# Kernel tuning notes

Hardware: AMD Instinct MI355X
Metric: run time of the kernel (lower is better)

The kernel has to match this reference:

```python
import jax, jax.numpy as jnp
import numpy as np

D_MODEL = 1024
NUM_HEADS = 16
HEAD_DIM = D_MODEL // NUM_HEADS
B, T_Q, T_KV = 4, 4096, 4096


def setup_inputs() -> dict:
    key = jax.random.key(0)
    ks = jax.random.split(key, 10)
    s_in = 1.0 / np.sqrt(D_MODEL)
    s_out = 1.0 / np.sqrt(D_MODEL)
    return {
        "q": jax.random.normal(ks[0], (B, T_Q, D_MODEL), jnp.float32),
        "kv": jax.random.normal(ks[1], (B, T_KV, D_MODEL), jnp.float32),
        # per-head projection weights stacked: [H, d_model, head_dim]
        "Wq": jax.random.uniform(ks[2], (NUM_HEADS, D_MODEL, HEAD_DIM), jnp.float32, -s_in, s_in),
        "bq": jax.random.uniform(ks[3], (NUM_HEADS, HEAD_DIM), jnp.float32, -s_in, s_in),
        "Wk": jax.random.uniform(ks[4], (NUM_HEADS, D_MODEL, HEAD_DIM), jnp.float32, -s_in, s_in),
        "bk": jax.random.uniform(ks[5], (NUM_HEADS, HEAD_DIM), jnp.float32, -s_in, s_in),
        "Wv": jax.random.uniform(ks[6], (NUM_HEADS, D_MODEL, HEAD_DIM), jnp.float32, -s_in, s_in),
        "bv": jax.random.uniform(ks[7], (NUM_HEADS, HEAD_DIM), jnp.float32, -s_in, s_in),
        "Wo": jax.random.uniform(ks[8], (D_MODEL, D_MODEL), jnp.float32, -s_out, s_out),
        "bo": jax.random.uniform(ks[9], (D_MODEL,), jnp.float32, -s_out, s_out),
    }


def reference(q, kv, Wq, bq, Wk, bk, Wv, bv, Wo, bo):
    Bsz, Tq, _ = q.shape
    # per-head projections fused into one batched GEMM each: [b,t,d] x [h,d,e] -> [b,h,t,e]
    qh = jnp.einsum('btd,hde->bhte', q, Wq) + bq[None, :, None, :]
    kh = jnp.einsum('btd,hde->bhte', kv, Wk) + bk[None, :, None, :]
    vh = jnp.einsum('btd,hde->bhte', kv, Wv) + bv[None, :, None, :]
    # squared feature map
    qh = qh * qh
    kh = kh * kh
    # O(N) linear attention aggregation
    kv_sum = jnp.einsum('bhnd,bhne->bhde', kh, vh)           # [B,H,e,e]
    z = 1.0 / (jnp.einsum('bhnd,bhd->bhn', qh, kh.sum(axis=2)) + 1e-6)  # [B,H,Tq]
    attn = jnp.einsum('bhnd,bhde,bhn->bhne', qh, kv_sum, z)  # [B,H,Tq,e]
    attn = attn.transpose(0, 2, 1, 3).reshape(Bsz, Tq, D_MODEL)
    return attn @ Wo.T + bo
```

## Files before the change

### kernel.cpp

```cpp
#include <hip/hip_runtime.h>

#define BSZ 4
#define TSEQ 4096
#define DM 1024
#define NH 16
#define HD 64
#define BT (BSZ * TSEQ)
#define INV_LOSCALE (1.0f / 4096.0f)

using f32x4 = __attribute__((ext_vector_type(4))) float;
using f16x8 = __attribute__((ext_vector_type(8))) _Float16;
using u32x2 = __attribute__((ext_vector_type(2))) unsigned;
using u32x4 = __attribute__((ext_vector_type(4))) unsigned;

typedef const __attribute__((address_space(1))) void* gas_ptr;
typedef __attribute__((address_space(3))) void* las_ptr;

__device__ __forceinline__ void gload16(const void* g, void* l) {
    __builtin_amdgcn_global_load_lds((gas_ptr)g, (las_ptr)l, 16, 0, 0);
}

__device__ __forceinline__ void split1(float x, _Float16& h, _Float16& l) {
    h = (_Float16)x;
    l = (_Float16)((x - (float)h) * 4096.0f);
}
__device__ __forceinline__ unsigned pack2(_Float16 a, _Float16 b) {
    return (unsigned)__builtin_bit_cast(unsigned short, a) |
           ((unsigned)__builtin_bit_cast(unsigned short, b) << 16);
}
__device__ __forceinline__ f32x4 mfma_f16(f16x8 a, f16x8 b, f32x4 c) {
    return __builtin_amdgcn_mfma_f32_16x16x32_f16(a, b, c, 0, 0, 0);
}

__global__ __launch_bounds__(256) void fragsplit_kernel(const float* __restrict__ in,
        _Float16* __restrict__ hi, _Float16* __restrict__ lo) {
    const int C = blockIdx.x * 256 + threadIdx.x;
    const int l15 = C & 15, quad = (C >> 4) & 3, rb = (C >> 6) & 3;
    const int s = (C >> 8) & 31, panel = C >> 13;
    const size_t src = ((size_t)(panel * 64 + rb * 16 + l15)) * DM + s * 32 + quad * 8;
    f32x4 v0 = *(const f32x4*)&in[src];
    f32x4 v1 = *(const f32x4*)&in[src + 4];
    _Float16 h[8], l[8];
    #pragma unroll
    for (int j = 0; j < 4; ++j) { split1(v0[j], h[j], l[j]); split1(v1[j], h[4 + j], l[4 + j]); }
    ((u32x4*)hi)[C] = (u32x4){pack2(h[0],h[1]), pack2(h[2],h[3]), pack2(h[4],h[5]), pack2(h[6],h[7])};
    ((u32x4*)lo)[C] = (u32x4){pack2(l[0],l[1]), pack2(l[2],l[3]), pack2(l[4],l[5]), pack2(l[6],l[7])};
}

__global__ __launch_bounds__(256) void wsplit_kernel(
    const float* __restrict__ Wq, const float* __restrict__ Wk, const float* __restrict__ Wv,
    _Float16* __restrict__ qh, _Float16* __restrict__ ql,
    _Float16* __restrict__ kh, _Float16* __restrict__ kl,
    _Float16* __restrict__ vh, _Float16* __restrict__ vl) {
    const int tid = threadIdx.x;
    const int k0 = blockIdx.x * 64, h = blockIdx.y, w = blockIdx.z;
    const float* __restrict__ W = (w == 0) ? Wq : (w == 1) ? Wk : Wv;
    _Float16* __restrict__ dh = (w == 0) ? qh : (w == 1) ? kh : vh;
    _Float16* __restrict__ dl = (w == 0) ? ql : (w == 1) ? kl : vl;
    __shared__ __align__(16) float ws_[64][68];
    #pragma unroll
    for (int it = 0; it < 4; ++it) {
        int idx = it * 256 + tid;
        int r = idx >> 4, c4 = (idx & 15) * 4;
        *(f32x4*)&ws_[r][c4] = *(const f32x4*)&W[((size_t)h * DM + k0 + r) * HD + c4];
    }
    __syncthreads();
    const int n = tid >> 2, kq16 = (tid & 3) * 16;
    _Float16 hh[16], ll[16];
    #pragma unroll
    for (int j = 0; j < 16; ++j) split1(ws_[kq16 + j][n], hh[j], ll[j]);
    #pragma unroll
    for (int c = 0; c < 2; ++c) {
        int kg = k0 + kq16 + c * 8;
        int s = kg >> 5, quad = (kg >> 3) & 3;
        size_t chunk = (size_t)(h * 32 + s) * 256 + ((n >> 4) * 4 + quad) * 16 + (n & 15);
        ((u32x4*)dh)[chunk] = (u32x4){pack2(hh[c*8+0],hh[c*8+1]), pack2(hh[c*8+2],hh[c*8+3]),
                                      pack2(hh[c*8+4],hh[c*8+5]), pack2(hh[c*8+6],hh[c*8+7])};
        ((u32x4*)dl)[chunk] = (u32x4){pack2(ll[c*8+0],ll[c*8+1]), pack2(ll[c*8+2],ll[c*8+3]),
                                      pack2(ll[c*8+4],ll[c*8+5]), pack2(ll[c*8+6],ll[c*8+7])};
    }
}

__global__ __launch_bounds__(256, 2) void kv_stats_kernel(
    const _Float16* __restrict__ kv_hi, const _Float16* __restrict__ kv_lo,
    const _Float16* __restrict__ wkt_hi, const _Float16* __restrict__ wkt_lo,
    const _Float16* __restrict__ wvt_hi, const _Float16* __restrict__ wvt_lo,
    const float* __restrict__ bk, const float* __restrict__ bv,
    float* __restrict__ kv_sum, float* __restrict__ ksum)
{
    const int tid = threadIdx.x;
    const int lane = tid & 63, wave = tid >> 6, quad = lane >> 4, l15 = lane & 15;
    const int b = blockIdx.z, h = blockIdx.y, bx = blockIdx.x;

    __shared__ __align__(16) char smem[65536];
    _Float16* khT_h = (_Float16*)smem;
    _Float16* khT_l = (_Float16*)(smem + 16384);
    _Float16* vhT_h = (_Float16*)(smem + 32768);
    _Float16* vhT_l = (_Float16*)(smem + 49152);

    const int isV = wave >> 1, half = wave & 1;
    const size_t btile = (size_t)h * 32;

    f32x4 racc_h[4] = {}, racc_c[4] = {};
    f32x4 rk_h = {}, rk_c = {};
    const f16x8 ones = __builtin_bit_cast(f16x8,
        (u32x4){0x3C003C00u, 0x3C003C00u, 0x3C003C00u, 0x3C003C00u});

    for (int sub = 0; sub < 2; ++sub) {
        const size_t apan = (size_t)(b * 64 + bx * 4 + sub * 2);
        auto stage = [&](int p, int s) {
            char* dst = smem + p * 32768 + tid * 16;
            const size_t a0 = (apan * 32 + s) * 2048 + tid * 8;
            const size_t a1 = ((apan + 1) * 32 + s) * 2048 + tid * 8;
            const size_t bo = (btile + s) * 2048 + tid * 8;
            gload16(&kv_hi[a0], dst);
            gload16(&kv_hi[a1], dst + 4096);
            gload16(&kv_lo[a0], dst + 8192);
            gload16(&kv_lo[a1], dst + 12288);
            gload16(&wkt_hi[bo], dst + 16384);
            gload16(&wkt_lo[bo], dst + 20480);
            gload16(&wvt_hi[bo], dst + 24576);
            gload16(&wvt_lo[bo], dst + 28672);
        };

        f32x4 acc_h[4][4] = {}, acc_c[4][4] = {};
        stage(0, 0);
        for (int s = 0; s < 32; ++s) {
            const int p = s & 1;
            if (s < 31) {
                stage(p ^ 1, s + 1);
                asm volatile("s_waitcnt vmcnt(8)" ::: "memory");
            } else {
                asm volatile("s_waitcnt vmcnt(0)" ::: "memory");
            }
            __builtin_amdgcn_s_barrier();
            __builtin_amdgcn_sched_barrier(0);
            const char* bufc = smem + p * 32768;
            const _Float16* a_hi = (const _Float16*)bufc;
            const _Float16* a_lo = (const _Float16*)(bufc + 8192);
            const _Float16* bh = (const _Float16*)(bufc + (isV ? 24576 : 16384));
            const _Float16* bl = (const _Float16*)(bufc + (isV ? 28672 : 20480));
            f16x8 afh[4], afl[4], bfh[4], bfl[4];
            #pragma unroll
            for (int mt = 0; mt < 4; ++mt) {
                afh[mt] = *(const f16x8*)&a_hi[half * 2048 + mt * 512 + lane * 8];
                afl[mt] = *(const f16x8*)&a_lo[half * 2048 + mt * 512 + lane * 8];
            }
            #pragma unroll
            for (int nt = 0; nt < 4; ++nt) {
                bfh[nt] = *(const f16x8*)&bh[nt * 512 + lane * 8];
                bfl[nt] = *(const f16x8*)&bl[nt * 512 + lane * 8];
            }
            #pragma unroll
            for (int mt = 0; mt < 4; ++mt)
                #pragma unroll
                for (int nt = 0; nt < 4; ++nt) {
                    acc_h[mt][nt] = mfma_f16(afh[mt], bfh[nt], acc_h[mt][nt]);
                    acc_c[mt][nt] = mfma_f16(afh[mt], bfl[nt], acc_c[mt][nt]);
                    acc_c[mt][nt] = mfma_f16(afl[mt], bfh[nt], acc_c[mt][nt]);
                }
            __builtin_amdgcn_s_barrier();
            __builtin_amdgcn_sched_barrier(0);
        }

        {
            const float* __restrict__ bias = (isV ? bv : bk) + h * HD;
            _Float16* __restrict__ dh = isV ? vhT_h : khT_h;
            _Float16* __restrict__ dl = isV ? vhT_l : khT_l;
            float bia[4];
            #pragma unroll
            for (int nt = 0; nt < 4; ++nt) bia[nt] = bias[nt * 16 + l15];
            #pragma unroll
            for (int mt = 0; mt < 4; ++mt) {
                const int S = half * 2 + (mt >> 1);
                const int tq = (mt & 1) * 2 + (quad >> 1);
                const int eo = (quad & 1) * 4;
                #pragma unroll
                for (int nt = 0; nt < 4; ++nt) {
                    _Float16 hh[4], ll[4];
                    #pragma unroll
                    for (int r = 0; r < 4; ++r) {
                        float v = acc_h[mt][nt][r] + INV_LOSCALE * acc_c[mt][nt][r] + bia[nt];
                        if (!isV) v = v * v;
                        split1(v, hh[r], ll[r]);
                    }
                    int fo = S * 2048 + (nt * 4 + tq) * 128 + l15 * 8 + eo;
                    *(u32x2*)&dh[fo] = (u32x2){pack2(hh[0], hh[1]), pack2(hh[2], hh[3])};
                    *(u32x2*)&dl[fo] = (u32x2){pack2(ll[0], ll[1]), pack2(ll[2], ll[3])};
                }
            }
        }
        __syncthreads();

        #pragma unroll
        for (int S = 0; S < 4; ++S) {
            f16x8 ah = *(const f16x8*)&khT_h[S * 2048 + wave * 512 + lane * 8];
            f16x8 al = *(const f16x8*)&khT_l[S * 2048 + wave * 512 + lane * 8];
            rk_h = mfma_f16(ah, ones, rk_h);
            rk_c = mfma_f16(al, ones, rk_c);
            #pragma unroll
            for (int nt = 0; nt < 4; ++nt) {
                f16x8 bh = *(const f16x8*)&vhT_h[S * 2048 + nt * 512 + lane * 8];
                f16x8 bl = *(const f16x8*)&vhT_l[S * 2048 + nt * 512 + lane * 8];
                racc_h[nt] = mfma_f16(ah, bh, racc_h[nt]);
                racc_c[nt] = mfma_f16(ah, bl, racc_c[nt]);
                racc_c[nt] = mfma_f16(al, bh, racc_c[nt]);
            }
        }
        __syncthreads();
    }

    float* kvp = kv_sum + (size_t)(b * NH + h) * HD * HD;
    #pragma unroll
    for (int nt = 0; nt < 4; ++nt)
        #pragma unroll
        for (int r = 0; r < 4; ++r)
            atomicAdd(&kvp[(wave * 16 + quad * 4 + r) * HD + nt * 16 + l15],
                      racc_h[nt][r] + INV_LOSCALE * racc_c[nt][r]);
    if (l15 == 0) {
        float* ksp = ksum + (b * NH + h) * HD;
        #pragma unroll
        for (int r = 0; r < 4; ++r)
            atomicAdd(&ksp[wave * 16 + quad * 4 + r], rk_h[r] + INV_LOSCALE * rk_c[r]);
    }
}

__global__ __launch_bounds__(256) void pmat_kernel(
    const float* __restrict__ kv_sum, const float* __restrict__ Wo,
    _Float16* __restrict__ pt_hi, _Float16* __restrict__ pt_lo)
{
    const int tid = threadIdx.x;
    const int opan = blockIdx.x, h = blockIdx.y, b = blockIdx.z;
    __shared__ __align__(16) float kvsT[64][68];
    __shared__ __align__(16) float wos[64][68];
    const float* __restrict__ kvp = kv_sum + (size_t)(b * NH + h) * HD * HD;
    #pragma unroll
    for (int it = 0; it < 4; ++it) {
        int idx = it * 256 + tid;
        int d = idx >> 4, e4 = (idx & 15) * 4;
        f32x4 v = *(const f32x4*)&kvp[d * HD + e4];
        kvsT[e4 + 0][d] = v.x; kvsT[e4 + 1][d] = v.y;
        kvsT[e4 + 2][d] = v.z; kvsT[e4 + 3][d] = v.w;
        int o = idx >> 4;
        *(f32x4*)&wos[o][e4] = *(const f32x4*)&Wo[(size_t)(opan * 64 + o) * DM + h * HD + e4];
    }
    __syncthreads();
    const int ty = tid >> 4, tx = tid & 15;
    f32x4 sv[4] = {};
    #pragma unroll 8
    for (int e = 0; e < 64; ++e) {
        f32x4 kv4 = *(const f32x4*)&kvsT[e][tx * 4];
        #pragma unroll
        for (int i = 0; i < 4; ++i) sv[i] += wos[ty * 4 + i][e] * kv4;
    }
    const int d0 = tx * 4;
    const int S = h * 2 + (d0 >> 5);
    const int kq = (d0 >> 3) & 3;
    const int rem8 = (d0 & 4) ? 8 : 0;
    #pragma unroll
    for (int i = 0; i < 4; ++i) {
        int ol = ty * 4 + i;
        f32x4 o4 = sv[i] * INV_LOSCALE;
        _Float16 hh[4], ll[4];
        #pragma unroll
        for (int j = 0; j < 4; ++j) split1(o4[j], hh[j], ll[j]);
        size_t cb = ((((size_t)(b * 16 + opan) * 32 + S) * 256 +
                      ((ol >> 4) * 4 + kq) * 16 + (ol & 15)) << 4) + rem8;
        *(u32x2*)((char*)pt_hi + cb) = (u32x2){pack2(hh[0], hh[1]), pack2(hh[2], hh[3])};
        *(u32x2*)((char*)pt_lo + cb) = (u32x2){pack2(ll[0], ll[1]), pack2(ll[2], ll[3])};
    }
}

__global__ __launch_bounds__(256, 3) void q_attn_ps_kernel(
    const _Float16* __restrict__ qf_hi, const _Float16* __restrict__ qf_lo,
    const _Float16* __restrict__ wqt_hi, const _Float16* __restrict__ wqt_lo,
    const float* __restrict__ bq, const float* __restrict__ ksum,
    _Float16* __restrict__ attn_hi, _Float16* __restrict__ attn_lo)
{
    const int tid = threadIdx.x;
    const int lane = tid & 63, wave = tid >> 6, quad = lane >> 4, l15 = lane & 15;
    const int b = blockIdx.z, h = blockIdx.y, bx = blockIdx.x;

    __shared__ __align__(16) char smem[49152];
    __shared__ float z_s[128], ks_s[64];

    if (tid < 64) ks_s[tid] = ksum[(b * NH + h) * HD + tid];

    const size_t apan = (size_t)(b * 64 + bx * 2);
    const size_t btile = (size_t)h * 32;

    auto stage = [&](int p, int s) {
        char* dst = smem + p * 24576 + tid * 16;
        const size_t a0 = (apan * 32 + s) * 2048 + tid * 8;
        const size_t a1 = ((apan + 1) * 32 + s) * 2048 + tid * 8;
        const size_t bo = (btile + s) * 2048 + tid * 8;
        gload16(&qf_hi[a0], dst);
        gload16(&qf_hi[a1], dst + 4096);
        gload16(&qf_lo[a0], dst + 8192);
        gload16(&qf_lo[a1], dst + 12288);
        gload16(&wqt_hi[bo], dst + 16384);
        gload16(&wqt_lo[bo], dst + 20480);
    };

    f32x4 acc_h[2][4] = {}, acc_c[2][4] = {};
    stage(0, 0);
    for (int s = 0; s < 32; ++s) {
        const int p = s & 1;
        if (s < 31) {
            stage(p ^ 1, s + 1);
            asm volatile("s_waitcnt vmcnt(6)" ::: "memory");
        } else {
            asm volatile("s_waitcnt vmcnt(0)" ::: "memory");
        }
        __builtin_amdgcn_s_barrier();
        __builtin_amdgcn_sched_barrier(0);
        const char* bufc = smem + p * 24576;
        const _Float16* a_hi = (const _Float16*)bufc;
        const _Float16* a_lo = (const _Float16*)(bufc + 8192);
        f16x8 afh[2], afl[2], bfh[4], bfl[4];
        #pragma unroll
        for (int mt = 0; mt < 2; ++mt) {
            int fo = (wave * 2 + mt) * 512 + lane * 8;
            afh[mt] = *(const f16x8*)&a_hi[fo];
            afl[mt] = *(const f16x8*)&a_lo[fo];
        }
        #pragma unroll
        for (int nt = 0; nt < 4; ++nt) {
            bfh[nt] = *(const f16x8*)((const _Float16*)(bufc + 16384) + nt * 512 + lane * 8);
            bfl[nt] = *(const f16x8*)((const _Float16*)(bufc + 20480) + nt * 512 + lane * 8);
        }
        #pragma unroll
        for (int mt = 0; mt < 2; ++mt)
            #pragma unroll
            for (int nt = 0; nt < 4; ++nt) {
                acc_h[mt][nt] = mfma_f16(afh[mt], bfh[nt], acc_h[mt][nt]);
                acc_c[mt][nt] = mfma_f16(afh[mt], bfl[nt], acc_c[mt][nt]);
                acc_c[mt][nt] = mfma_f16(afl[mt], bfh[nt], acc_c[mt][nt]);
            }
        __builtin_amdgcn_s_barrier();
        __builtin_amdgcn_sched_barrier(0);
    }

    float* qs = (float*)smem;
    {
        const float* __restrict__ bias = bq + h * HD;
        float zp[2][4] = {};
        #pragma unroll
        for (int nt = 0; nt < 4; ++nt) {
            int d = nt * 16 + l15;
            float bia = bias[d];
            float ks  = ks_s[d];
            #pragma unroll
            for (int mt = 0; mt < 2; ++mt)
                #pragma unroll
                for (int r = 0; r < 4; ++r) {
                    int t = wave * 32 + mt * 16 + quad * 4 + r;
                    float v = acc_h[mt][nt][r] + INV_LOSCALE * acc_c[mt][nt][r] + bia;
                    float v2 = v * v;
                    qs[t * 68 + d] = v2;
                    zp[mt][r] = fmaf(v2, ks, zp[mt][r]);
                }
        }
        #pragma unroll
        for (int mt = 0; mt < 2; ++mt)
            #pragma unroll
            for (int r = 0; r < 4; ++r) {
                float p = zp[mt][r];
                p += __shfl_xor(p, 1);
                p += __shfl_xor(p, 2);
                p += __shfl_xor(p, 4);
                p += __shfl_xor(p, 8);
                if (l15 == 0) z_s[wave * 32 + mt * 16 + quad * 4 + r] = 4096.0f / (p + 1e-6f);
            }
    }
    __syncthreads();

    #pragma unroll
    for (int it = 0; it < 4; ++it) {
        int cid = it * 256 + tid;
        int lp = cid >> 9, Sl = (cid >> 8) & 1, c = cid & 255;
        int t = lp * 64 + (c >> 6) * 16 + (c & 15);
        int d = Sl * 32 + ((c >> 4) & 3) * 8;
        f32x4 a0 = *(const f32x4*)&qs[t * 68 + d];
        f32x4 a1 = *(const f32x4*)&qs[t * 68 + d + 4];
        float z = z_s[t];
        _Float16 hh[8], ll[8];
        #pragma unroll
        for (int j = 0; j < 4; ++j) {
            split1(z * a0[j], hh[j], ll[j]);
            split1(z * a1[j], hh[4 + j], ll[4 + j]);
        }
        size_t cb = (((size_t)(b * 64 + bx * 2 + lp) * 32 + h * 2 + Sl) * 256 + c) << 4;
        *(u32x4*)((char*)attn_hi + cb) =
            (u32x4){pack2(hh[0],hh[1]), pack2(hh[2],hh[3]), pack2(hh[4],hh[5]), pack2(hh[6],hh[7])};
        *(u32x4*)((char*)attn_lo + cb) =
            (u32x4){pack2(ll[0],ll[1]), pack2(ll[2],ll[3]), pack2(ll[4],ll[5]), pack2(ll[6],ll[7])};
    }
}

__global__ __launch_bounds__(256, 3) void q_attn_kernel(
    const float* __restrict__ q,
    const _Float16* __restrict__ wqt_hi, const _Float16* __restrict__ wqt_lo,
    const float* __restrict__ bq,
    const float* __restrict__ kv_sum, const float* __restrict__ ksum,
    _Float16* __restrict__ attn_hi, _Float16* __restrict__ attn_lo)
{
    const int tid = threadIdx.x;
    const int lane = tid & 63, wave = tid >> 6, quad = lane >> 4, l15 = lane & 15;
    const int b = blockIdx.z, h = blockIdx.y, bx = blockIdx.x;
    const int t0 = bx * 64;

    __shared__ __align__(16) char smem[32768];
    __shared__ __align__(16) float qs[64 * 68];
    __shared__ float z_s[64], ks_s[64];

    if (tid < 64) ks_s[tid] = ksum[(b * NH + h) * HD + tid];

    const int arb = tid >> 6, aquad = (tid >> 4) & 3, al15 = tid & 15;
    const float* __restrict__ qrow =
        q + ((size_t)b * TSEQ + t0 + arb * 16 + al15) * DM + aquad * 8;
    const size_t btile = (size_t)h * 32;

    auto asplit_write = [&](int p, f32x4 v0, f32x4 v1) {
        _Float16 hh[8], ll[8];
        #pragma unroll
        for (int j = 0; j < 4; ++j) { split1(v0[j], hh[j], ll[j]); split1(v1[j], hh[4+j], ll[4+j]); }
        char* dst = smem + p * 16384 + tid * 16;
        *(u32x4*)dst =
            (u32x4){pack2(hh[0],hh[1]), pack2(hh[2],hh[3]), pack2(hh[4],hh[5]), pack2(hh[6],hh[7])};
        *(u32x4*)(dst + 4096) =
            (u32x4){pack2(ll[0],ll[1]), pack2(ll[2],ll[3]), pack2(ll[4],ll[5]), pack2(ll[6],ll[7])};
    };
    auto stageB = [&](int p, int s) {
        char* dst = smem + p * 16384 + 8192 + tid * 16;
        const size_t bo = (btile + s) * 2048 + tid * 8;
        gload16(&wqt_hi[bo], dst);
        gload16(&wqt_lo[bo], dst + 4096);
    };

    f32x4 acc_h[4] = {}, acc_c[4] = {};
    f32x4 v0 = *(const f32x4*)&qrow[0];
    f32x4 v1 = *(const f32x4*)&qrow[4];
    asplit_write(0, v0, v1);
    stageB(0, 0);
    v0 = *(const f32x4*)&qrow[32];
    v1 = *(const f32x4*)&qrow[36];
    asm volatile("s_waitcnt vmcnt(2) lgkmcnt(0)" ::: "memory");
    __builtin_amdgcn_s_barrier();
    __builtin_amdgcn_sched_barrier(0);

    for (int s = 0; s < 32; ++s) {
        const int p = s & 1;
        if (s < 31) {
            stageB(p ^ 1, s + 1);
            asplit_write(p ^ 1, v0, v1);
            if (s < 30) {
                v0 = *(const f32x4*)&qrow[(s + 2) * 32];
                v1 = *(const f32x4*)&qrow[(s + 2) * 32 + 4];
            }
            asm volatile("s_waitcnt vmcnt(4) lgkmcnt(0)" ::: "memory");
        } else {
            asm volatile("s_waitcnt vmcnt(0)" ::: "memory");
        }
        __builtin_amdgcn_s_barrier();
        __builtin_amdgcn_sched_barrier(0);
        const char* bufc = smem + p * 16384;
        f16x8 afh = *(const f16x8*)((const _Float16*)bufc + wave * 512 + lane * 8);
        f16x8 afl = *(const f16x8*)((const _Float16*)(bufc + 4096) + wave * 512 + lane * 8);
        f16x8 bfh[4], bfl[4];
        #pragma unroll
        for (int nt = 0; nt < 4; ++nt) {
            bfh[nt] = *(const f16x8*)((const _Float16*)(bufc + 8192) + nt * 512 + lane * 8);
            bfl[nt] = *(const f16x8*)((const _Float16*)(bufc + 12288) + nt * 512 + lane * 8);
        }
        #pragma unroll
        for (int nt = 0; nt < 4; ++nt) {
            acc_h[nt] = mfma_f16(afh, bfh[nt], acc_h[nt]);
            acc_c[nt] = mfma_f16(afh, bfl[nt], acc_c[nt]);
            acc_c[nt] = mfma_f16(afl, bfh[nt], acc_c[nt]);
        }
        __builtin_amdgcn_s_barrier();
        __builtin_amdgcn_sched_barrier(0);
    }

    {
        const int mrow0 = wave * 16;
        const float* __restrict__ bias = bq + h * HD;
        float zp[4] = {0.f, 0.f, 0.f, 0.f};
        #pragma unroll
        for (int nt = 0; nt < 4; ++nt) {
            int d = nt * 16 + l15;
            float bia = bias[d];
            float ks  = ks_s[d];
            #pragma unroll
            for (int r = 0; r < 4; ++r) {
                int t = mrow0 + quad * 4 + r;
                float v = acc_h[nt][r] + INV_LOSCALE * acc_c[nt][r] + bia;
                float v2 = v * v;
                qs[t * 68 + d] = v2;
                zp[r] = fmaf(v2, ks, zp[r]);
            }
        }
        #pragma unroll
        for (int r = 0; r < 4; ++r) {
            float p = zp[r];
            p += __shfl_xor(p, 1);
            p += __shfl_xor(p, 2);
            p += __shfl_xor(p, 4);
            p += __shfl_xor(p, 8);
            if (l15 == 0) z_s[mrow0 + quad * 4 + r] = 1.f / (p + 1e-6f);
        }
    }
    __syncthreads();

    float* kvs = (float*)smem;
    {
        const float* __restrict__ kvp = kv_sum + (size_t)(b * NH + h) * HD * HD;
        #pragma unroll
        for (int it = 0; it < 4; ++it) {
            int idx = it * 256 + tid;
            int r = idx >> 4, c = (idx & 15) * 4;
            *(f32x4*)&kvs[r * 64 + c] = *(const f32x4*)&kvp[r * HD + c];
        }
    }
    __syncthreads();

    const int ty = tid >> 4, tx = tid & 15;
    f32x4 sv[4] = {};
    #pragma unroll 4
    for (int d = 0; d < 64; d += 4) {
        f32x4 b0 = *(const f32x4*)&kvs[(d + 0) * 64 + tx * 4];
        f32x4 b1 = *(const f32x4*)&kvs[(d + 1) * 64 + tx * 4];
        f32x4 b2 = *(const f32x4*)&kvs[(d + 2) * 64 + tx * 4];
        f32x4 b3 = *(const f32x4*)&kvs[(d + 3) * 64 + tx * 4];
        #pragma unroll
        for (int i = 0; i < 4; ++i) {
            f32x4 av = *(const f32x4*)&qs[(ty * 4 + i) * 68 + d];
            sv[i] += av.x * b0 + av.y * b1 + av.z * b2 + av.w * b3;
        }
    }
    const size_t opanel = (size_t)b * 64 + bx;
    const int s_out = h * 2 + (tx >> 3);
    const int kq = (tx >> 1) & 3;
    const int rem8 = (tx & 1) * 8;
    #pragma unroll
    for (int i = 0; i < 4; ++i) {
        int t = ty * 4 + i;
        f32x4 o = sv[i] * z_s[t];
        _Float16 hh[4], ll[4];
        #pragma unroll
        for (int j = 0; j < 4; ++j) split1(o[j], hh[j], ll[j]);
        size_t cb = (((opanel * 32 + s_out) * 256 + ((t >> 4) * 4 + kq) * 16 + (t & 15)) << 4) + rem8;
        *(u32x2*)((char*)attn_hi + cb) = (u32x2){pack2(hh[0], hh[1]), pack2(hh[2], hh[3])};
        *(u32x2*)((char*)attn_lo + cb) = (u32x2){pack2(ll[0], ll[1]), pack2(ll[2], ll[3])};
    }
}

__global__ __launch_bounds__(256, 3) void out_proj_p_kernel(
    const _Float16* __restrict__ attn_hi, const _Float16* __restrict__ attn_lo,
    const _Float16* __restrict__ pt_hi, const _Float16* __restrict__ pt_lo,
    const float* __restrict__ bo, float* __restrict__ out)
{
    const int tid = threadIdx.x;
    const int lane = tid & 63, wave = tid >> 6, quad = lane >> 4, l15 = lane & 15;
    const int n0 = blockIdx.x * 64;
    const size_t m0 = (size_t)blockIdx.y * 128;

    __shared__ __align__(16) char smem[49152];
    float* cs = (float*)smem;

    const size_t ap0 = (m0 >> 6) * 32, ap1 = ap0 + 32;
    const int bb = (int)(m0 >> 12);
    const _Float16* __restrict__ pbh = pt_hi + (size_t)bb * 16 * 32 * 2048;
    const _Float16* __restrict__ pbl = pt_lo + (size_t)bb * 16 * 32 * 2048;
    const size_t bpn = (size_t)(n0 >> 6) * 32;

    auto stage = [&](int p, int s) {
        char* dst = smem + p * 24576 + tid * 16;
        const size_t co = (size_t)s * 2048 + tid * 8;
        gload16(&attn_hi[ap0 * 2048 + co], dst);
        gload16(&attn_hi[ap1 * 2048 + co], dst + 4096);
        gload16(&attn_lo[ap0 * 2048 + co], dst + 8192);
        gload16(&attn_lo[ap1 * 2048 + co], dst + 12288);
        gload16(&pbh[(bpn + s) * 2048 + tid * 8], dst + 16384);
        gload16(&pbl[(bpn + s) * 2048 + tid * 8], dst + 20480);
    };

    const int panel = wave >> 1;
    f32x4 acc_h[2][4] = {}, acc_c[2][4] = {};
    stage(0, 0);
    for (int s = 0; s < 32; ++s) {
        const int p = s & 1;
        if (s < 31) {
            stage(p ^ 1, s + 1);
            asm volatile("s_waitcnt vmcnt(6)" ::: "memory");
        } else {
            asm volatile("s_waitcnt vmcnt(0)" ::: "memory");
        }
        __builtin_amdgcn_s_barrier();
        __builtin_amdgcn_sched_barrier(0);
        const char* bufc = smem + p * 24576;
        f16x8 afh[2], afl[2], bfh[4], bfl[4];
        #pragma unroll
        for (int mt = 0; mt < 2; ++mt) {
            int rbl = (wave & 1) * 2 + mt;
            afh[mt] = *(const f16x8*)((const _Float16*)(bufc + panel * 4096) + rbl * 512 + lane * 8);
            afl[mt] = *(const f16x8*)((const _Float16*)(bufc + 8192 + panel * 4096) + rbl * 512 + lane * 8);
        }
        #pragma unroll
        for (int nt = 0; nt < 4; ++nt) {
            bfh[nt] = *(const f16x8*)((const _Float16*)(bufc + 16384) + nt * 512 + lane * 8);
            bfl[nt] = *(const f16x8*)((const _Float16*)(bufc + 20480) + nt * 512 + lane * 8);
        }
        #pragma unroll
        for (int mt = 0; mt < 2; ++mt)
            #pragma unroll
            for (int nt = 0; nt < 4; ++nt) {
                acc_h[mt][nt] = mfma_f16(afh[mt], bfh[nt], acc_h[mt][nt]);
                acc_c[mt][nt] = mfma_f16(afh[mt], bfl[nt], acc_c[mt][nt]);
                acc_c[mt][nt] = mfma_f16(afl[mt], bfh[nt], acc_c[mt][nt]);
            }
        __builtin_amdgcn_s_barrier();
        __builtin_amdgcn_sched_barrier(0);
    }

    {
        float bia[4];
        #pragma unroll
        for (int nt = 0; nt < 4; ++nt) bia[nt] = bo[n0 + nt * 16 + l15];
        #pragma unroll
        for (int mt = 0; mt < 2; ++mt)
            #pragma unroll
            for (int nt = 0; nt < 4; ++nt)
                #pragma unroll
                for (int r = 0; r < 4; ++r) {
                    int t = wave * 32 + mt * 16 + quad * 4 + r;
                    cs[t * 64 + nt * 16 + l15] =
                        acc_h[mt][nt][r] + INV_LOSCALE * acc_c[mt][nt][r] + bia[nt];
                }
    }
    __syncthreads();
    #pragma unroll
    for (int it = 0; it < 8; ++it) {
        int idx = it * 256 + tid;
        int r = idx >> 4, c = (idx & 15) * 4;
        *(f32x4*)&out[(m0 + r) * DM + n0 + c] = *(f32x4*)&cs[r * 64 + c];
    }
}

__global__ __launch_bounds__(256, 3) void out_proj_kernel(
    const _Float16* __restrict__ attn_hi, const _Float16* __restrict__ attn_lo,
    const _Float16* __restrict__ wo_hi, const _Float16* __restrict__ wo_lo,
    const float* __restrict__ bo, float* __restrict__ out)
{
    const int tid = threadIdx.x;
    const int lane = tid & 63, wave = tid >> 6, quad = lane >> 4, l15 = lane & 15;
    const int n0 = blockIdx.x * 64;
    const size_t m0 = (size_t)blockIdx.y * 128;

    __shared__ __align__(16) char smem[49152];
    float* cs = (float*)smem;

    const size_t ap0 = (m0 >> 6) * 32, ap1 = ap0 + 32;
    const size_t bpn = (size_t)(n0 >> 6) * 32;

    auto stage = [&](int p, int s) {
        char* dst = smem + p * 24576 + tid * 16;
        const size_t co = (size_t)s * 2048 + tid * 8;
        gload16(&attn_hi[ap0 * 2048 + co], dst);
        gload16(&attn_hi[ap1 * 2048 + co], dst + 4096);
        gload16(&attn_lo[ap0 * 2048 + co], dst + 8192);
        gload16(&attn_lo[ap1 * 2048 + co], dst + 12288);
        gload16(&wo_hi[(bpn + s) * 2048 + tid * 8], dst + 16384);
        gload16(&wo_lo[(bpn + s) * 2048 + tid * 8], dst + 20480);
    };

    const int panel = wave >> 1;
    f32x4 acc_h[2][4] = {}, acc_c[2][4] = {};
    stage(0, 0);
    for (int s = 0; s < 32; ++s) {
        const int p = s & 1;
        if (s < 31) {
            stage(p ^ 1, s + 1);
            asm volatile("s_waitcnt vmcnt(6)" ::: "memory");
        } else {
            asm volatile("s_waitcnt vmcnt(0)" ::: "memory");
        }
        __builtin_amdgcn_s_barrier();
        __builtin_amdgcn_sched_barrier(0);
        const char* bufc = smem + p * 24576;
        f16x8 afh[2], afl[2], bfh[4], bfl[4];
        #pragma unroll
        for (int mt = 0; mt < 2; ++mt) {
            int rbl = (wave & 1) * 2 + mt;
            afh[mt] = *(const f16x8*)((const _Float16*)(bufc + panel * 4096) + rbl * 512 + lane * 8);
            afl[mt] = *(const f16x8*)((const _Float16*)(bufc + 8192 + panel * 4096) + rbl * 512 + lane * 8);
        }
        #pragma unroll
        for (int nt = 0; nt < 4; ++nt) {
            bfh[nt] = *(const f16x8*)((const _Float16*)(bufc + 16384) + nt * 512 + lane * 8);
            bfl[nt] = *(const f16x8*)((const _Float16*)(bufc + 20480) + nt * 512 + lane * 8);
        }
        #pragma unroll
        for (int mt = 0; mt < 2; ++mt)
            #pragma unroll
            for (int nt = 0; nt < 4; ++nt) {
                acc_h[mt][nt] = mfma_f16(afh[mt], bfh[nt], acc_h[mt][nt]);
                acc_c[mt][nt] = mfma_f16(afh[mt], bfl[nt], acc_c[mt][nt]);
                acc_c[mt][nt] = mfma_f16(afl[mt], bfh[nt], acc_c[mt][nt]);
            }
        __builtin_amdgcn_s_barrier();
        __builtin_amdgcn_sched_barrier(0);
    }

    {
        float bia[4];
        #pragma unroll
        for (int nt = 0; nt < 4; ++nt) bia[nt] = bo[n0 + nt * 16 + l15];
        #pragma unroll
        for (int mt = 0; mt < 2; ++mt)
            #pragma unroll
            for (int nt = 0; nt < 4; ++nt)
                #pragma unroll
                for (int r = 0; r < 4; ++r) {
                    int t = wave * 32 + mt * 16 + quad * 4 + r;
                    cs[t * 64 + nt * 16 + l15] =
                        acc_h[mt][nt][r] + INV_LOSCALE * acc_c[mt][nt][r] + bia[nt];
                }
    }
    __syncthreads();
    #pragma unroll
    for (int it = 0; it < 8; ++it) {
        int idx = it * 256 + tid;
        int r = idx >> 4, c = (idx & 15) * 4;
        *(f32x4*)&out[(m0 + r) * DM + n0 + c] = *(f32x4*)&cs[r * 64 + c];
    }
}

extern "C" void kernel_launch(void* const* d_in, const int* in_sizes, int n_in,
                              void* d_out, int out_size, void* d_ws, size_t ws_size,
                              hipStream_t stream) {
    const float* q  = (const float*)d_in[0];
    const float* kv = (const float*)d_in[1];
    const float* Wq = (const float*)d_in[2];
    const float* bq = (const float*)d_in[3];
    const float* Wk = (const float*)d_in[4];
    const float* bk = (const float*)d_in[5];
    const float* Wv = (const float*)d_in[6];
    const float* bv = (const float*)d_in[7];
    const float* Wo = (const float*)d_in[8];
    const float* bo = (const float*)d_in[9];
    float* out = (float*)d_out;

    char* p = (char*)d_ws;
    float* kv_sum = (float*)p;              p += (size_t)BSZ * NH * HD * HD * 4;
    float* ksum   = (float*)p;              p += (size_t)BSZ * NH * HD * 4;
    _Float16* wqt_hi = (_Float16*)p;        p += (size_t)NH * HD * DM * 2;
    _Float16* wqt_lo = (_Float16*)p;        p += (size_t)NH * HD * DM * 2;
    _Float16* wkt_hi = (_Float16*)p;        p += (size_t)NH * HD * DM * 2;
    _Float16* wkt_lo = (_Float16*)p;        p += (size_t)NH * HD * DM * 2;
    _Float16* wvt_hi = (_Float16*)p;        p += (size_t)NH * HD * DM * 2;
    _Float16* wvt_lo = (_Float16*)p;        p += (size_t)NH * HD * DM * 2;
    _Float16* wo_hi  = (_Float16*)p;        p += (size_t)DM * DM * 2;
    _Float16* wo_lo  = (_Float16*)p;        p += (size_t)DM * DM * 2;
    _Float16* buf_hi = (_Float16*)p;        p += (size_t)BT * DM * 2;
    _Float16* buf_lo = (_Float16*)p;        p += (size_t)BT * DM * 2;
    _Float16* qf_hi  = (_Float16*)p;        p += (size_t)BT * DM * 2;
    _Float16* qf_lo  = (_Float16*)p;        p += (size_t)BT * DM * 2;
    _Float16* pt_hi  = (_Float16*)p;        p += (size_t)BSZ * DM * DM * 2;
    _Float16* pt_lo  = (_Float16*)p;        p += (size_t)BSZ * DM * DM * 2;
    const bool big = ws_size >= (size_t)(p - (char*)d_ws);

    size_t zero_bytes = ((size_t)BSZ * NH * HD * HD + (size_t)BSZ * NH * HD) * sizeof(float);
    hipMemsetAsync(d_ws, 0, zero_bytes, stream);

    fragsplit_kernel<<<(BT * DM / 8) / 256, 256, 0, stream>>>(kv, buf_hi, buf_lo);
    wsplit_kernel<<<dim3(DM / 64, NH, 3), 256, 0, stream>>>(
        Wq, Wk, Wv, wqt_hi, wqt_lo, wkt_hi, wkt_lo, wvt_hi, wvt_lo);
    if (!big)
        fragsplit_kernel<<<(DM * DM / 8) / 256, 256, 0, stream>>>(Wo, wo_hi, wo_lo);

    kv_stats_kernel<<<dim3(TSEQ / 256, NH, BSZ), 256, 0, stream>>>(
        buf_hi, buf_lo, wkt_hi, wkt_lo, wvt_hi, wvt_lo, bk, bv, kv_sum, ksum);

    if (big) {
        fragsplit_kernel<<<(BT * DM / 8) / 256, 256, 0, stream>>>(q, qf_hi, qf_lo);
        pmat_kernel<<<dim3(16, NH, BSZ), 256, 0, stream>>>(kv_sum, Wo, pt_hi, pt_lo);
        q_attn_ps_kernel<<<dim3(TSEQ / 128, NH, BSZ), 256, 0, stream>>>(
            qf_hi, qf_lo, wqt_hi, wqt_lo, bq, ksum, buf_hi, buf_lo);
        out_proj_p_kernel<<<dim3(DM / 64, BT / 128), 256, 0, stream>>>(
            buf_hi, buf_lo, pt_hi, pt_lo, bo, out);
    } else {
        q_attn_kernel<<<dim3(TSEQ / 64, NH, BSZ), 256, 0, stream>>>(
            q, wqt_hi, wqt_lo, bq, kv_sum, ksum, buf_hi, buf_lo);
        out_proj_kernel<<<dim3(DM / 64, BT / 128), 256, 0, stream>>>(
            buf_hi, buf_lo, wo_hi, wo_lo, bo, out);
    }
}
```

Before: 626.0 us.

## Drop low-half attention term in out-projection and remap blocks per XCD

The q_attn_ps kernel now writes only the fp16 high part of the normalized attention, and out_proj_p drops the attn_lo load and its correction MFMA. This cuts out-projection memory traffic, shared memory and MFMA work by about a third, and the kernel's occupancy hint rises to 4. All three main kernels also move to a 1D grid with an XCD-aware block index mapping, so blocks that share a head or N tile land on the same XCD for L2 reuse. The cost is lower precision on the attention operand, which relies on fp16 rounding of the attention values alone staying within tolerance.

```diff
diff --git a/kernel.cpp b/kernel.cpp
--- a/kernel.cpp
+++ b/kernel.cpp
@@ -90,7 +90,11 @@
 {
     const int tid = threadIdx.x;
     const int lane = tid & 63, wave = tid >> 6, quad = lane >> 4, l15 = lane & 15;
-    const int b = blockIdx.z, h = blockIdx.y, bx = blockIdx.x;
+    const int g = blockIdx.x;
+    const int xcd = g & 7, kk = g >> 3;
+    const int h = kk & 15, sg = kk >> 4;
+    const int strip = xcd + 8 * sg;
+    const int b = strip >> 4, bx = strip & 15;
 
     __shared__ __align__(16) char smem[65536];
     _Float16* khT_h = (_Float16*)smem;
@@ -275,11 +279,15 @@
     const _Float16* __restrict__ qf_hi, const _Float16* __restrict__ qf_lo,
     const _Float16* __restrict__ wqt_hi, const _Float16* __restrict__ wqt_lo,
     const float* __restrict__ bq, const float* __restrict__ ksum,
-    _Float16* __restrict__ attn_hi, _Float16* __restrict__ attn_lo)
+    _Float16* __restrict__ attn_hi)
 {
     const int tid = threadIdx.x;
     const int lane = tid & 63, wave = tid >> 6, quad = lane >> 4, l15 = lane & 15;
-    const int b = blockIdx.z, h = blockIdx.y, bx = blockIdx.x;
+    const int g = blockIdx.x;
+    const int xcd = g & 7, kk = g >> 3;
+    const int h = kk & 15, sg = kk >> 4;
+    const int strip = xcd + 8 * sg;
+    const int b = strip >> 5, bx = strip & 31;
 
     __shared__ __align__(16) char smem[49152];
     __shared__ float z_s[128], ks_s[64];
@@ -384,17 +392,15 @@
         f32x4 a0 = *(const f32x4*)&qs[t * 68 + d];
         f32x4 a1 = *(const f32x4*)&qs[t * 68 + d + 4];
         float z = z_s[t];
-        _Float16 hh[8], ll[8];
+        _Float16 hh[8];
         #pragma unroll
         for (int j = 0; j < 4; ++j) {
-            split1(z * a0[j], hh[j], ll[j]);
-            split1(z * a1[j], hh[4 + j], ll[4 + j]);
+            hh[j]     = (_Float16)(z * a0[j]);
+            hh[4 + j] = (_Float16)(z * a1[j]);
         }
         size_t cb = (((size_t)(b * 64 + bx * 2 + lp) * 32 + h * 2 + Sl) * 256 + c) << 4;
         *(u32x4*)((char*)attn_hi + cb) =
             (u32x4){pack2(hh[0],hh[1]), pack2(hh[2],hh[3]), pack2(hh[4],hh[5]), pack2(hh[6],hh[7])};
-        *(u32x4*)((char*)attn_lo + cb) =
-            (u32x4){pack2(ll[0],ll[1]), pack2(ll[2],ll[3]), pack2(ll[4],ll[5]), pack2(ll[6],ll[7])};
     }
 }
 
@@ -556,17 +562,21 @@
     }
 }
 
-__global__ __launch_bounds__(256, 3) void out_proj_p_kernel(
-    const _Float16* __restrict__ attn_hi, const _Float16* __restrict__ attn_lo,
+__global__ __launch_bounds__(256, 4) void out_proj_p_kernel(
+    const _Float16* __restrict__ attn_hi,
     const _Float16* __restrict__ pt_hi, const _Float16* __restrict__ pt_lo,
     const float* __restrict__ bo, float* __restrict__ out)
 {
     const int tid = threadIdx.x;
     const int lane = tid & 63, wave = tid >> 6, quad = lane >> 4, l15 = lane & 15;
-    const int n0 = blockIdx.x * 64;
-    const size_t m0 = (size_t)blockIdx.y * 128;
-
-    __shared__ __align__(16) char smem[49152];
+    const int g = blockIdx.x;
+    const int xcd = g & 7, kk = g >> 3;
+    const int nidx = kk & 15, sg = kk >> 4;
+    const int mstrip = xcd + 8 * sg;
+    const int n0 = nidx * 64;
+    const size_t m0 = (size_t)mstrip * 128;
+
+    __shared__ __align__(16) char smem[32768];
     float* cs = (float*)smem;
 
     const size_t ap0 = (m0 >> 6) * 32, ap1 = ap0 + 32;
@@ -576,14 +586,12 @@
     const size_t bpn = (size_t)(n0 >> 6) * 32;
 
     auto stage = [&](int p, int s) {
-        char* dst = smem + p * 24576 + tid * 16;
+        char* dst = smem + p * 16384 + tid * 16;
         const size_t co = (size_t)s * 2048 + tid * 8;
         gload16(&attn_hi[ap0 * 2048 + co], dst);
         gload16(&attn_hi[ap1 * 2048 + co], dst + 4096);
-        gload16(&attn_lo[ap0 * 2048 + co], dst + 8192);
-        gload16(&attn_lo[ap1 * 2048 + co], dst + 12288);
-        gload16(&pbh[(bpn + s) * 2048 + tid * 8], dst + 16384);
-        gload16(&pbl[(bpn + s) * 2048 + tid * 8], dst + 20480);
+        gload16(&pbh[(bpn + s) * 2048 + tid * 8], dst + 8192);
+        gload16(&pbl[(bpn + s) * 2048 + tid * 8], dst + 12288);
     };
 
     const int panel = wave >> 1;
@@ -593,24 +601,23 @@
         const int p = s & 1;
         if (s < 31) {
             stage(p ^ 1, s + 1);
-            asm volatile("s_waitcnt vmcnt(6)" ::: "memory");
+            asm volatile("s_waitcnt vmcnt(4)" ::: "memory");
         } else {
             asm volatile("s_waitcnt vmcnt(0)" ::: "memory");
         }
         __builtin_amdgcn_s_barrier();
         __builtin_amdgcn_sched_barrier(0);
-        const char* bufc = smem + p * 24576;
-        f16x8 afh[2], afl[2], bfh[4], bfl[4];
+        const char* bufc = smem + p * 16384;
+        f16x8 afh[2], bfh[4], bfl[4];
         #pragma unroll
         for (int mt = 0; mt < 2; ++mt) {
             int rbl = (wave & 1) * 2 + mt;
             afh[mt] = *(const f16x8*)((const _Float16*)(bufc + panel * 4096) + rbl * 512 + lane * 8);
-            afl[mt] = *(const f16x8*)((const _Float16*)(bufc + 8192 + panel * 4096) + rbl * 512 + lane * 8);
         }
         #pragma unroll
         for (int nt = 0; nt < 4; ++nt) {
-            bfh[nt] = *(const f16x8*)((const _Float16*)(bufc + 16384) + nt * 512 + lane * 8);
-            bfl[nt] = *(const f16x8*)((const _Float16*)(bufc + 20480) + nt * 512 + lane * 8);
+            bfh[nt] = *(const f16x8*)((const _Float16*)(bufc + 8192) + nt * 512 + lane * 8);
+            bfl[nt] = *(const f16x8*)((const _Float16*)(bufc + 12288) + nt * 512 + lane * 8);
         }
         #pragma unroll
         for (int mt = 0; mt < 2; ++mt)
@@ -618,7 +625,6 @@
             for (int nt = 0; nt < 4; ++nt) {
                 acc_h[mt][nt] = mfma_f16(afh[mt], bfh[nt], acc_h[mt][nt]);
                 acc_c[mt][nt] = mfma_f16(afh[mt], bfl[nt], acc_c[mt][nt]);
-                acc_c[mt][nt] = mfma_f16(afl[mt], bfh[nt], acc_c[mt][nt]);
             }
         __builtin_amdgcn_s_barrier();
         __builtin_amdgcn_sched_barrier(0);
@@ -780,16 +786,16 @@
     if (!big)
         fragsplit_kernel<<<(DM * DM / 8) / 256, 256, 0, stream>>>(Wo, wo_hi, wo_lo);
 
-    kv_stats_kernel<<<dim3(TSEQ / 256, NH, BSZ), 256, 0, stream>>>(
+    kv_stats_kernel<<<NH * (TSEQ / 256) * BSZ, 256, 0, stream>>>(
         buf_hi, buf_lo, wkt_hi, wkt_lo, wvt_hi, wvt_lo, bk, bv, kv_sum, ksum);
 
     if (big) {
         fragsplit_kernel<<<(BT * DM / 8) / 256, 256, 0, stream>>>(q, qf_hi, qf_lo);
         pmat_kernel<<<dim3(16, NH, BSZ), 256, 0, stream>>>(kv_sum, Wo, pt_hi, pt_lo);
-        q_attn_ps_kernel<<<dim3(TSEQ / 128, NH, BSZ), 256, 0, stream>>>(
-            qf_hi, qf_lo, wqt_hi, wqt_lo, bq, ksum, buf_hi, buf_lo);
-        out_proj_p_kernel<<<dim3(DM / 64, BT / 128), 256, 0, stream>>>(
-            buf_hi, buf_lo, pt_hi, pt_lo, bo, out);
+        q_attn_ps_kernel<<<NH * (TSEQ / 128) * BSZ, 256, 0, stream>>>(
+            qf_hi, qf_lo, wqt_hi, wqt_lo, bq, ksum, buf_hi);
+        out_proj_p_kernel<<<(DM / 64) * (BT / 128), 256, 0, stream>>>(
+            buf_hi, pt_hi, pt_lo, bo, out);
     } else {
         q_attn_kernel<<<dim3(TSEQ / 64, NH, BSZ), 256, 0, stream>>>(
             q, wqt_hi, wqt_lo, bq, kv_sum, ksum, buf_hi, buf_lo);
```

Measured after the change: 606.5 us. 1.03x faster.
